# Optimization experiments

Measured on AMD Instinct MI355X. Metric: run time of the kernel, lower is better.

Reference implementation:

```python
import jax, jax.numpy as jnp
import numpy as np

GRID = 30
S = GRID * GRID            # 900 cells
D = 512                    # embed_dim
HQ = 8                     # query heads
HKV = 2                    # kv heads (GQA)
DH = D // HQ               # 64 head dim
T = 16                     # history length


def _rope_pairwise_1d(x, pos, inv_freq):
    """RoPE on adjacent pairs. x: (L,H,d), pos: (L,), inv_freq: (d//2,)."""
    theta = pos[:, None] * inv_freq[None, :]          # (L, d//2)
    cos = jnp.cos(theta)[:, None, :]                  # (L,1,d//2)
    sin = jnp.sin(theta)[:, None, :]
    xr, xi = x[..., 0::2], x[..., 1::2]               # even/odd pairs (= view(L,H,-1,2))
    out = jnp.stack((xr * cos - xi * sin, xr * sin + xi * cos), axis=-1)
    return out.reshape(x.shape)


def _rope_2d(x, coords_xy, inv_x, inv_y):
    """2D RoPE: first half rotated by x-coord, second half by y-coord."""
    d_axis = x.shape[-1] // 2
    x_part = _rope_pairwise_1d(x[..., :d_axis], coords_xy[:, 0], inv_x)
    y_part = _rope_pairwise_1d(x[..., d_axis:], coords_xy[:, 1], inv_y)
    return jnp.concatenate((x_part, y_part), axis=-1)


def setup_inputs() -> dict:
    key = jax.random.key(0)
    ks = jax.random.split(key, 7)
    sc = 1.0 / np.sqrt(D)
    return {
        "static_grid": jax.random.normal(ks[0], (GRID, GRID, D), jnp.float32),
        "history_seq": jax.random.normal(ks[1], (T, GRID, GRID, D), jnp.float32),
        "init_embed": jax.random.normal(ks[2], (D,), jnp.float32),
        "Wq": jax.random.normal(ks[3], (D, D), jnp.float32) * sc,
        "Wk": jax.random.normal(ks[4], (HKV * DH, D), jnp.float32) * sc,
        "Wv": jax.random.normal(ks[5], (HKV * DH, D), jnp.float32) * sc,
        "Wo": jax.random.normal(ks[6], (D, D), jnp.float32) * sc,
    }


def reference(static_grid, history_seq, init_embed, Wq, Wk, Wv, Wo):
    dtype = static_grid.dtype
    quarter, half = DH // 4, DH // 2
    inv_2d = 1.0 / (10000.0 ** (jnp.arange(quarter, dtype=dtype) / quarter))  # (dh//4,)
    inv_1d = 1.0 / (10000.0 ** (jnp.arange(half, dtype=dtype) / half))        # (dh//2,)

    gy, gx = jnp.meshgrid(jnp.arange(GRID), jnp.arange(GRID), indexing="ij")
    coords = jnp.stack((gy, gx), axis=-1).reshape(S, 2).astype(dtype)          # (S,2)

    cur = static_grid.reshape(S, D)                    # current frame tokens
    hist = history_seq.reshape(T * S, D)               # per-cell histories
    # token order: [learnable_init, cell_histories (t=0..T-1), current_grid]
    tokens = jnp.concatenate((init_embed[None, :], hist, cur), axis=0)  # (Lkv, D)

    tok_pos = jnp.concatenate((
        jnp.zeros((1,), dtype),
        jnp.repeat(jnp.arange(T, dtype=dtype), S),
        jnp.full((S,), T, dtype=dtype),
    ))                                                  # (Lkv,) temporal positions
    tok_coords = jnp.concatenate((
        jnp.zeros((1, 2), dtype),
        jnp.tile(coords, (T, 1)),
        coords,
    ), axis=0)                                          # (Lkv,2)

    # projections (queries only for the current frame; output is the updated frame)
    q = (cur @ Wq.T).reshape(S, HQ, DH)
    k = (tokens @ Wk.T).reshape(-1, HKV, DH)
    v = (tokens @ Wv.T).reshape(-1, HKV, DH)

    # fused temporal(1D) + spatial(2D) RoPE on q and k
    q = _rope_2d(_rope_pairwise_1d(q, jnp.full((S,), T, dtype=dtype), inv_1d), coords, inv_2d, inv_2d)
    k = _rope_2d(_rope_pairwise_1d(k, tok_pos, inv_1d), tok_coords, inv_2d, inv_2d)

    # grouped-query attention: expand kv heads
    g = HQ // HKV
    k = jnp.repeat(k, g, axis=1)                        # (Lkv, HQ, DH)
    v = jnp.repeat(v, g, axis=1)

    scores = jnp.einsum("qhd,khd->hqk", q, k) / jnp.sqrt(jnp.asarray(DH, dtype))

    # pedestal mask: attend to init + own temporal column + all current cells
    cell = jnp.arange(S)
    hist_cell = jnp.tile(cell, T)                       # (T*S,)
    mask = jnp.concatenate((
        jnp.ones((S, 1), bool),
        cell[:, None] == hist_cell[None, :],
        jnp.ones((S, S), bool),
    ), axis=1)                                          # (S, Lkv)
    scores = jnp.where(mask[None], scores, jnp.finfo(dtype).min)

    attn = jax.nn.softmax(scores, axis=-1)
    out = jnp.einsum("hqk,khd->qhd", attn, v).reshape(S, D)
    return (out @ Wo.T).reshape(GRID, GRID, D)
```

## Files before the change

### kernel.cpp

```cpp
#include <hip/hip_runtime.h>
#include <math.h>

static constexpr int GRIDN = 30;
static constexpr int S    = 900;
static constexpr int D    = 512;
static constexpr int HQ   = 8;
static constexpr int HKV  = 2;
static constexpr int T    = 16;
static constexpr int NTOK = 1 + T*S + S;
static constexpr int CUR0 = 1 + T*S;

static constexpr int THROWS = 15360;
static constexpr int VTC    = 960;
static constexpr int PBS    = 952;

typedef _Float16 half8 __attribute__((ext_vector_type(8)));
typedef _Float16 half4 __attribute__((ext_vector_type(4)));
typedef float    floatx4 __attribute__((ext_vector_type(4)));

#define MFMA16(a,b,c) __builtin_amdgcn_mfma_f32_16x16x32_f16((a),(b),(c),0,0,0)

__device__ __forceinline__ half8 to_half8(float4 a, float4 b) {
    half8 h;
    h[0]=(_Float16)a.x; h[1]=(_Float16)a.y; h[2]=(_Float16)a.z; h[3]=(_Float16)a.w;
    h[4]=(_Float16)b.x; h[5]=(_Float16)b.y; h[6]=(_Float16)b.z; h[7]=(_Float16)b.w;
    return h;
}

__global__ __launch_bounds__(256) void prep(
    const float* __restrict__ Wq, const float* __restrict__ Wk,
    const float* __restrict__ Wv, const float* __restrict__ Wo,
    const float* __restrict__ init_e, const float* __restrict__ hist,
    const float* __restrict__ cur,
    _Float16* __restrict__ Wqh, _Float16* __restrict__ Whkv,
    _Float16* __restrict__ Woh, _Float16* __restrict__ Th)
{
    const size_t i8 = ((size_t)blockIdx.x * 256 + threadIdx.x) * 8;
    const float* src; _Float16* dst; size_t off;
    if (i8 < 262144)      { src = Wq; dst = Wqh;          off = i8; }
    else if (i8 < 327680) { src = Wk; dst = Whkv;         off = i8 - 262144; }
    else if (i8 < 393216) { src = Wv; dst = Whkv + 65536; off = i8 - 327680; }
    else if (i8 < 655360) { src = Wo; dst = Woh;          off = i8 - 393216; }
    else {
        const size_t o = i8 - 655360;
        if (o >= (size_t)NTOK * 512) return;
        dst = Th; off = o;
        if (o < 512)                    src = init_e;
        else if (o < (size_t)CUR0*512)  { src = hist; dst = Th + 512; off = o - 512; }
        else                            { src = cur;  dst = Th + (size_t)CUR0*512; off = o - (size_t)CUR0*512; }
    }
    const float4 f0 = *(const float4*)(src + off);
    const float4 f1 = *(const float4*)(src + off + 4);
    *(half8*)(dst + off) = to_half8(f0, f1);
}

__global__ __launch_bounds__(256) void proj(
    const _Float16* __restrict__ Th, const _Float16* __restrict__ Whkv,
    const _Float16* __restrict__ Wqh,
    _Float16* __restrict__ Kh, _Float16* __restrict__ Vh,
    _Float16* __restrict__ Vt, _Float16* __restrict__ Qh)
{
    const int tid = threadIdx.x;
    const int w = tid >> 6, lane = tid & 63;
    const int r = lane & 15, kb = lane >> 4;
    const int bx = blockIdx.x;
    const bool isQ = (bx >= 479);

    int l0, n0;
    const _Float16* B;
    if (!isQ) { l0 = bx * 32; B = Whkv; n0 = 0; }
    else {
        const int qb = bx - 479;
        l0 = CUR0 + (qb >> 1) * 32;
        B = Wqh; n0 = (qb & 1) * 256;
    }

    const _Float16* ap[2];
    #pragma unroll
    for (int mt = 0; mt < 2; ++mt) {
        int l = l0 + mt*16 + r;
        if (l >= NTOK) l = 0;
        ap[mt] = Th + (size_t)l * 512 + kb*8;
    }
    const _Float16* bp[4];
    #pragma unroll
    for (int nt = 0; nt < 4; ++nt)
        bp[nt] = B + (size_t)(n0 + w*64 + nt*16 + r) * 512 + kb*8;

    floatx4 acc[2][4] = {};
    #pragma unroll 2
    for (int k0 = 0; k0 < 512; k0 += 32) {
        half8 a[2], b[4];
        #pragma unroll
        for (int mt = 0; mt < 2; ++mt) a[mt] = *(const half8*)(ap[mt] + k0);
        #pragma unroll
        for (int nt = 0; nt < 4; ++nt) b[nt] = *(const half8*)(bp[nt] + k0);
        #pragma unroll
        for (int mt = 0; mt < 2; ++mt)
            #pragma unroll
            for (int nt = 0; nt < 4; ++nt)
                acc[mt][nt] = MFMA16(a[mt], b[nt], acc[mt][nt]);
    }

    const float LN1E4 = 9.210340371976184f;
    float inv1[4], inv2[4]; int jj[4];
    #pragma unroll
    for (int nt = 0; nt < 4; ++nt) {
        const int cl = nt*16 + r;
        jj[nt] = cl >> 1;
        inv1[nt] = __expf(-(float)jj[nt]        * (LN1E4 / 32.f));
        inv2[nt] = __expf(-(float)(jj[nt] & 15) * (LN1E4 / 16.f));
    }

    if (!isQ) {
        if (w < 2) {
            #pragma unroll
            for (int mt = 0; mt < 2; ++mt)
                #pragma unroll
                for (int i = 0; i < 4; ++i) {
                    const int l = l0 + mt*16 + kb*4 + i;
                    float pos, cy, cx;
                    if (l == 0) { pos = 0.f; cy = 0.f; cx = 0.f; }
                    else if (l <= T*S) {
                        const int j2 = l - 1;
                        const int t_ = j2 / S;
                        const int cell = j2 - t_ * S;
                        pos = (float)t_;
                        cy = (float)(cell / GRIDN); cx = (float)(cell % GRIDN);
                    } else {
                        const int cell = l - CUR0;
                        pos = (float)T;
                        cy = (float)(cell / GRIDN); cx = (float)(cell % GRIDN);
                    }
                    #pragma unroll
                    for (int nt = 0; nt < 4; ++nt) {
                        const float own = acc[mt][nt][i];
                        const float oth = __shfl_xor(own, 1);
                        const float c2 = (jj[nt] < 16) ? cy : cx;
                        const float theta = pos * inv1[nt] + c2 * inv2[nt];
                        float sn, cs; __sincosf(theta, &sn, &cs);
                        const int cl = nt*16 + r;
                        const float o = ((cl & 1) == 0) ? (own * cs - oth * sn)
                                                        : (oth * sn + own * cs);
                        if (l < NTOK) Kh[(size_t)l * 128 + w*64 + cl] = (_Float16)o;
                    }
                }
        } else {
            #pragma unroll
            for (int mt = 0; mt < 2; ++mt)
                #pragma unroll
                for (int nt = 0; nt < 4; ++nt) {
                    const int d = nt*16 + r;
                    #pragma unroll
                    for (int i = 0; i < 4; ++i) {
                        const int l = l0 + mt*16 + kb*4 + i;
                        if (l >= NTOK) continue;
                        const _Float16 hv = (_Float16)acc[mt][nt][i];
                        Vh[(size_t)l * 128 + (w-2)*64 + d] = hv;
                        const int cc = l - CUR0;
                        if (cc >= 0 && cc < S)
                            Vt[((size_t)(w-2)*64 + d) * VTC + cc] = hv;
                    }
                }
        }
    } else {
        #pragma unroll
        for (int mt = 0; mt < 2; ++mt)
            #pragma unroll
            for (int i = 0; i < 4; ++i) {
                const int l = l0 + mt*16 + kb*4 + i;
                const int s = l - CUR0;
                const float cy = (float)(s / GRIDN), cx = (float)(s % GRIDN);
                #pragma unroll
                for (int nt = 0; nt < 4; ++nt) {
                    const float own = acc[mt][nt][i];
                    const float oth = __shfl_xor(own, 1);
                    const float c2 = (jj[nt] < 16) ? cy : cx;
                    const float theta = 16.f * inv1[nt] + c2 * inv2[nt];
                    float sn, cs; __sincosf(theta, &sn, &cs);
                    const int cl = nt*16 + r;
                    const float o = ((cl & 1) == 0) ? (own * cs - oth * sn)
                                                    : (oth * sn + own * cs);
                    if (s < S)
                        Qh[(size_t)s * 512 + n0 + w*64 + cl] = (_Float16)(o * 0.125f);
                }
            }
    }
}

__global__ __launch_bounds__(256) void attn_f16(
    const _Float16* __restrict__ Qh, const _Float16* __restrict__ Kh,
    const _Float16* __restrict__ Vt, const _Float16* __restrict__ Vh,
    _Float16* __restrict__ Oh)
{
    __shared__ _Float16 pb[16][PBS];
    __shared__ float ex[16][20];
    __shared__ float wpm[4][16], wps[4][16];
    __shared__ float rowm[16], rowinv[16];
    __shared__ float Oe[16][68];

    const int q0  = blockIdx.x * 16;
    const int h   = blockIdx.y;
    const int kvh = h >> 2;
    const int tid = threadIdx.x;
    const int w = tid >> 6, lane = tid & 63;
    const int r = lane & 15, g = lane >> 4;

    {
        const int er = tid & 15;
        const int s  = q0 + er;
        const int ss = (s < S) ? s : 0;
        const _Float16* qp = Qh + (size_t)(q0 + er) * 512 + h * 64;
        for (int e = tid >> 4; e < 17; e += 16) {
            const int l = (e == 0) ? 0 : (1 + (e - 1) * S + ss);
            const _Float16* kp = Kh + (size_t)l * 128 + kvh * 64;
            float acc = 0.f;
            #pragma unroll
            for (int d8 = 0; d8 < 8; ++d8) {
                const half8 qv = *(const half8*)(qp + d8 * 8);
                const half8 kv = *(const half8*)(kp + d8 * 8);
                #pragma unroll
                for (int q_ = 0; q_ < 8; ++q_)
                    acc += (float)qv[q_] * (float)kv[q_];
            }
            ex[er][e] = acc;
        }
    }

    half8 qa[2];
    #pragma unroll
    for (int ks = 0; ks < 2; ++ks)
        qa[ks] = *(const half8*)(Qh + (size_t)(q0 + r) * 512 + h * 64 + ks * 32 + g * 8);

    floatx4 qacc[15];
    #pragma unroll
    for (int t = 0; t < 15; ++t) {
        const int nt = w + 4 * t;
        floatx4 a = {0.f, 0.f, 0.f, 0.f};
        if (nt <= 56) {
            const _Float16* kp = Kh + (size_t)(CUR0 + nt * 16 + r) * 128 + kvh * 64 + g * 8;
            a = MFMA16(qa[0], *(const half8*)kp, a);
            a = MFMA16(qa[1], *(const half8*)(kp + 32), a);
        }
        qacc[t] = a;
    }

    float pm[4] = {-1e30f, -1e30f, -1e30f, -1e30f};
    #pragma unroll
    for (int t = 0; t < 15; ++t) {
        const int nt = w + 4 * t;
        const bool valid = (nt <= 56) && !((nt == 56) && (r >= 4));
        #pragma unroll
        for (int i = 0; i < 4; ++i)
            if (valid) pm[i] = fmaxf(pm[i], qacc[t][i]);
    }
    #pragma unroll
    for (int m = 1; m < 16; m <<= 1)
        #pragma unroll
        for (int i = 0; i < 4; ++i)
            pm[i] = fmaxf(pm[i], __shfl_xor(pm[i], m));
    if (r == 0)
        #pragma unroll
        for (int i = 0; i < 4; ++i) wpm[w][g * 4 + i] = pm[i];
    __syncthreads();

    if (tid < 16) {
        float m = fmaxf(fmaxf(wpm[0][tid], wpm[1][tid]), fmaxf(wpm[2][tid], wpm[3][tid]));
        #pragma unroll
        for (int e = 0; e < 17; ++e) m = fmaxf(m, ex[tid][e]);
        rowm[tid] = m;
    }
    __syncthreads();

    {
        const int er = tid & 15;
        for (int e = tid >> 4; e < 17; e += 16)
            ex[er][e] = __expf(ex[er][e] - rowm[er]);
    }
    pb[tid >> 4][912 + (tid & 15)] = (_Float16)0.f;

    float ps[4] = {0.f, 0.f, 0.f, 0.f};
    #pragma unroll
    for (int t = 0; t < 15; ++t) {
        const int nt = w + 4 * t;
        if (nt <= 56) {
            const int c = nt * 16 + r;
            const bool masked = (nt == 56) && (r >= 4);
            #pragma unroll
            for (int i = 0; i < 4; ++i) {
                const int row = g * 4 + i;
                const float e = masked ? 0.f : __expf(qacc[t][i] - rowm[row]);
                ps[i] += e;
                pb[row][c] = (_Float16)e;
            }
        }
    }
    #pragma unroll
    for (int m = 1; m < 16; m <<= 1)
        #pragma unroll
        for (int i = 0; i < 4; ++i) ps[i] += __shfl_xor(ps[i], m);
    if (r == 0)
        #pragma unroll
        for (int i = 0; i < 4; ++i) wps[w][g * 4 + i] = ps[i];
    __syncthreads();

    if (tid < 16) {
        float s_ = wps[0][tid] + wps[1][tid] + wps[2][tid] + wps[3][tid];
        #pragma unroll
        for (int e = 0; e < 17; ++e) s_ += ex[tid][e];
        rowinv[tid] = 1.f / s_;
    }
    __syncthreads();

    {
        const int er = tid & 15, gg = tid >> 4;
        const int s  = q0 + er;
        const int ss = (s < S) ? s : 0;
        float o0 = 0.f, o1 = 0.f, o2 = 0.f, o3 = 0.f;
        for (int e = 0; e < 17; ++e) {
            const int l = (e == 0) ? 0 : (1 + (e - 1) * S + ss);
            const float p = ex[er][e];
            const half4 v = *(const half4*)(Vh + (size_t)l * 128 + kvh * 64 + gg * 4);
            o0 = fmaf(p, (float)v[0], o0); o1 = fmaf(p, (float)v[1], o1);
            o2 = fmaf(p, (float)v[2], o2); o3 = fmaf(p, (float)v[3], o3);
        }
        *(float4*)&Oe[er][gg * 4] = make_float4(o0, o1, o2, o3);
    }

    const int d0 = w * 16;
    floatx4 oa = {0.f, 0.f, 0.f, 0.f};
    const _Float16* vrow = Vt + ((size_t)kvh * 64 + d0 + r) * VTC + g * 8;
    #pragma unroll
    for (int ks = 0; ks < 29; ++ks) {
        const half8 pf = *(const half8*)(&pb[r][ks * 32 + g * 8]);
        const half8 vf = *(const half8*)(vrow + ks * 32);
        oa = MFMA16(pf, vf, oa);
    }
    __syncthreads();

    #pragma unroll
    for (int i = 0; i < 4; ++i) {
        const int row = g * 4 + i;
        const int s = q0 + row;
        if (s < S) {
            const float o = (oa[i] + Oe[row][d0 + r]) * rowinv[row];
            Oh[(size_t)s * 512 + h * 64 + d0 + r] = (_Float16)o;
        }
    }
}

__global__ __launch_bounds__(256) void gemm_out(
    const _Float16* __restrict__ A, const _Float16* __restrict__ Wh,
    float* __restrict__ Out, int M)
{
    const int tid = threadIdx.x;
    const int w = tid >> 6, lane = tid & 63;
    const int r = lane & 15, kb = lane >> 4;
    const int l0 = blockIdx.x * 32;
    const int n0 = blockIdx.y * 256 + w*64;

    const _Float16* ap[2];
    #pragma unroll
    for (int mt = 0; mt < 2; ++mt)
        ap[mt] = A + (size_t)(l0 + mt*16 + r)*512 + kb*8;
    const _Float16* bp[4];
    #pragma unroll
    for (int nt = 0; nt < 4; ++nt)
        bp[nt] = Wh + (size_t)(n0 + nt*16 + r) * 512 + kb*8;

    floatx4 acc[2][4] = {};
    #pragma unroll 2
    for (int k0 = 0; k0 < 512; k0 += 32) {
        half8 a[2], b[4];
        #pragma unroll
        for (int mt = 0; mt < 2; ++mt) a[mt] = *(const half8*)(ap[mt] + k0);
        #pragma unroll
        for (int nt = 0; nt < 4; ++nt) b[nt] = *(const half8*)(bp[nt] + k0);
        #pragma unroll
        for (int mt = 0; mt < 2; ++mt)
            #pragma unroll
            for (int nt = 0; nt < 4; ++nt)
                acc[mt][nt] = MFMA16(a[mt], b[nt], acc[mt][nt]);
    }
    #pragma unroll
    for (int mt = 0; mt < 2; ++mt)
        #pragma unroll
        for (int nt = 0; nt < 4; ++nt)
            #pragma unroll
            for (int i = 0; i < 4; ++i) {
                const int l = l0 + mt*16 + kb*4 + i;
                if (l < M)
                    Out[(size_t)l*512 + n0 + nt*16 + r] = acc[mt][nt][i];
            }
}

extern "C" void kernel_launch(void* const* d_in, const int* in_sizes, int n_in,
                              void* d_out, int out_size, void* d_ws, size_t ws_size,
                              hipStream_t stream)
{
    (void)in_sizes; (void)n_in; (void)out_size; (void)ws_size;
    const float* static_grid = (const float*)d_in[0];
    const float* history     = (const float*)d_in[1];
    const float* init_embed  = (const float*)d_in[2];
    const float* Wq = (const float*)d_in[3];
    const float* Wk = (const float*)d_in[4];
    const float* Wv = (const float*)d_in[5];
    const float* Wo = (const float*)d_in[6];
    float* out = (float*)d_out;

    char* p = (char*)d_ws;
    _Float16* Wqh  = (_Float16*)p;  p += (size_t)262144 * 2;
    _Float16* Whkv = (_Float16*)p;  p += (size_t)131072 * 2;
    _Float16* Woh  = (_Float16*)p;  p += (size_t)262144 * 2;
    _Float16* Th   = (_Float16*)p;  p += (size_t)THROWS * 512 * 2;
    _Float16* Kh   = (_Float16*)p;  p += (size_t)THROWS * 128 * 2;
    _Float16* Vh   = (_Float16*)p;  p += (size_t)THROWS * 128 * 2;
    _Float16* Vt   = (_Float16*)p;  p += (size_t)2 * 64 * VTC * 2;
    _Float16* Qh   = (_Float16*)p;  p += (size_t)928 * 512 * 2;
    _Float16* Oh   = (_Float16*)p;  p += (size_t)928 * 512 * 2;

    prep<<<4146, 256, 0, stream>>>(Wq, Wk, Wv, Wo, init_embed, history,
                                   static_grid, Wqh, Whkv, Woh, Th);
    proj<<<537, 256, 0, stream>>>(Th, Whkv, Wqh, Kh, Vh, Vt, Qh);
    attn_f16<<<dim3(57, 8), 256, 0, stream>>>(Qh, Kh, Vt, Vh, Oh);
    gemm_out<<<dim3(29, 2), 256, 0, stream>>>(Oh, Woh, out, S);
}
```

Before: 162.1 us.

## Fuse activation fp16 conversion into projection GEMM loads and drop Th buffer

The prep kernel now converts only weights; the projection GEMM reads fp32 token rows (init, history, current) directly and converts them to fp16 in registers with packed round-toward-zero conversion. This removes writing and re-reading a large fp16 token staging buffer. The exact-score dot products in attention use fdot2 when available. Round-toward-zero conversion slightly changes numerics versus round-to-nearest.

```diff
diff --git a/kernel.cpp b/kernel.cpp
--- a/kernel.cpp
+++ b/kernel.cpp
@@ -14,11 +14,18 @@
 static constexpr int VTC    = 960;
 static constexpr int PBS    = 952;
 
-typedef _Float16 half8 __attribute__((ext_vector_type(8)));
-typedef _Float16 half4 __attribute__((ext_vector_type(4)));
+typedef _Float16 half8  __attribute__((ext_vector_type(8)));
+typedef _Float16 half4  __attribute__((ext_vector_type(4)));
+typedef __fp16   fp16x2 __attribute__((ext_vector_type(2)));
 typedef float    floatx4 __attribute__((ext_vector_type(4)));
 
 #define MFMA16(a,b,c) __builtin_amdgcn_mfma_f32_16x16x32_f16((a),(b),(c),0,0,0)
+
+#if defined(__has_builtin)
+#if __has_builtin(__builtin_amdgcn_fdot2)
+#define HAVE_FDOT2 1
+#endif
+#endif
 
 __device__ __forceinline__ half8 to_half8(float4 a, float4 b) {
     half8 h;
@@ -27,36 +34,40 @@
     return h;
 }
 
-__global__ __launch_bounds__(256) void prep(
+__device__ __forceinline__ half8 cvt8(float4 a, float4 b) {
+    const fp16x2 p0 = __builtin_amdgcn_cvt_pkrtz(a.x, a.y);
+    const fp16x2 p1 = __builtin_amdgcn_cvt_pkrtz(a.z, a.w);
+    const fp16x2 p2 = __builtin_amdgcn_cvt_pkrtz(b.x, b.y);
+    const fp16x2 p3 = __builtin_amdgcn_cvt_pkrtz(b.z, b.w);
+    half8 h;
+    h[0]=(_Float16)p0[0]; h[1]=(_Float16)p0[1];
+    h[2]=(_Float16)p1[0]; h[3]=(_Float16)p1[1];
+    h[4]=(_Float16)p2[0]; h[5]=(_Float16)p2[1];
+    h[6]=(_Float16)p3[0]; h[7]=(_Float16)p3[1];
+    return h;
+}
+
+__global__ __launch_bounds__(256) void prep_w(
     const float* __restrict__ Wq, const float* __restrict__ Wk,
     const float* __restrict__ Wv, const float* __restrict__ Wo,
-    const float* __restrict__ init_e, const float* __restrict__ hist,
-    const float* __restrict__ cur,
     _Float16* __restrict__ Wqh, _Float16* __restrict__ Whkv,
-    _Float16* __restrict__ Woh, _Float16* __restrict__ Th)
+    _Float16* __restrict__ Woh)
 {
     const size_t i8 = ((size_t)blockIdx.x * 256 + threadIdx.x) * 8;
     const float* src; _Float16* dst; size_t off;
     if (i8 < 262144)      { src = Wq; dst = Wqh;          off = i8; }
     else if (i8 < 327680) { src = Wk; dst = Whkv;         off = i8 - 262144; }
     else if (i8 < 393216) { src = Wv; dst = Whkv + 65536; off = i8 - 327680; }
-    else if (i8 < 655360) { src = Wo; dst = Woh;          off = i8 - 393216; }
-    else {
-        const size_t o = i8 - 655360;
-        if (o >= (size_t)NTOK * 512) return;
-        dst = Th; off = o;
-        if (o < 512)                    src = init_e;
-        else if (o < (size_t)CUR0*512)  { src = hist; dst = Th + 512; off = o - 512; }
-        else                            { src = cur;  dst = Th + (size_t)CUR0*512; off = o - (size_t)CUR0*512; }
-    }
+    else                  { src = Wo; dst = Woh;          off = i8 - 393216; }
     const float4 f0 = *(const float4*)(src + off);
     const float4 f1 = *(const float4*)(src + off + 4);
     *(half8*)(dst + off) = to_half8(f0, f1);
 }
 
 __global__ __launch_bounds__(256) void proj(
-    const _Float16* __restrict__ Th, const _Float16* __restrict__ Whkv,
-    const _Float16* __restrict__ Wqh,
+    const float* __restrict__ init_e, const float* __restrict__ hist,
+    const float* __restrict__ cur,
+    const _Float16* __restrict__ Whkv, const _Float16* __restrict__ Wqh,
     _Float16* __restrict__ Kh, _Float16* __restrict__ Vh,
     _Float16* __restrict__ Vt, _Float16* __restrict__ Qh)
 {
@@ -75,12 +86,15 @@
         B = Wqh; n0 = (qb & 1) * 256;
     }
 
-    const _Float16* ap[2];
+    const float* ap[2];
     #pragma unroll
     for (int mt = 0; mt < 2; ++mt) {
         int l = l0 + mt*16 + r;
         if (l >= NTOK) l = 0;
-        ap[mt] = Th + (size_t)l * 512 + kb*8;
+        const float* row = (l == 0) ? init_e
+                         : (l <= T*S ? hist + (size_t)(l-1)*512
+                                     : cur  + (size_t)(l-CUR0)*512);
+        ap[mt] = row + kb*8;
     }
     const _Float16* bp[4];
     #pragma unroll
@@ -92,7 +106,11 @@
     for (int k0 = 0; k0 < 512; k0 += 32) {
         half8 a[2], b[4];
         #pragma unroll
-        for (int mt = 0; mt < 2; ++mt) a[mt] = *(const half8*)(ap[mt] + k0);
+        for (int mt = 0; mt < 2; ++mt) {
+            const float4 f0 = *(const float4*)(ap[mt] + k0);
+            const float4 f1 = *(const float4*)(ap[mt] + k0 + 4);
+            a[mt] = cvt8(f0, f1);
+        }
         #pragma unroll
         for (int nt = 0; nt < 4; ++nt) b[nt] = *(const half8*)(bp[nt] + k0);
         #pragma unroll
@@ -219,9 +237,18 @@
             for (int d8 = 0; d8 < 8; ++d8) {
                 const half8 qv = *(const half8*)(qp + d8 * 8);
                 const half8 kv = *(const half8*)(kp + d8 * 8);
+#ifdef HAVE_FDOT2
+                #pragma unroll
+                for (int p_ = 0; p_ < 4; ++p_) {
+                    fp16x2 qq; qq[0] = (__fp16)qv[2*p_]; qq[1] = (__fp16)qv[2*p_+1];
+                    fp16x2 kk; kk[0] = (__fp16)kv[2*p_]; kk[1] = (__fp16)kv[2*p_+1];
+                    acc = __builtin_amdgcn_fdot2(qq, kk, acc, false);
+                }
+#else
                 #pragma unroll
                 for (int q_ = 0; q_ < 8; ++q_)
                     acc += (float)qv[q_] * (float)kv[q_];
+#endif
             }
             ex[er][e] = acc;
         }
@@ -412,16 +439,15 @@
     _Float16* Wqh  = (_Float16*)p;  p += (size_t)262144 * 2;
     _Float16* Whkv = (_Float16*)p;  p += (size_t)131072 * 2;
     _Float16* Woh  = (_Float16*)p;  p += (size_t)262144 * 2;
-    _Float16* Th   = (_Float16*)p;  p += (size_t)THROWS * 512 * 2;
     _Float16* Kh   = (_Float16*)p;  p += (size_t)THROWS * 128 * 2;
     _Float16* Vh   = (_Float16*)p;  p += (size_t)THROWS * 128 * 2;
     _Float16* Vt   = (_Float16*)p;  p += (size_t)2 * 64 * VTC * 2;
     _Float16* Qh   = (_Float16*)p;  p += (size_t)928 * 512 * 2;
     _Float16* Oh   = (_Float16*)p;  p += (size_t)928 * 512 * 2;
 
-    prep<<<4146, 256, 0, stream>>>(Wq, Wk, Wv, Wo, init_embed, history,
-                                   static_grid, Wqh, Whkv, Woh, Th);
-    proj<<<537, 256, 0, stream>>>(Th, Whkv, Wqh, Kh, Vh, Vt, Qh);
+    prep_w<<<320, 256, 0, stream>>>(Wq, Wk, Wv, Wo, Wqh, Whkv, Woh);
+    proj<<<537, 256, 0, stream>>>(init_embed, history, static_grid,
+                                  Whkv, Wqh, Kh, Vh, Vt, Qh);
     attn_f16<<<dim3(57, 8), 256, 0, stream>>>(Qh, Kh, Vt, Vh, Oh);
     gemm_out<<<dim3(29, 2), 256, 0, stream>>>(Oh, Woh, out, S);
 }
```

Result: slower. 168.5 us (+3.9%).
